# Kernel optimization log

Hardware: AMD Instinct MI355X
Metric: run time of the kernel (lower is better)

## Reference

```python
import jax, jax.numpy as jnp
import numpy as np

B, S, D = 4, 512, 4096
H, G = 32, 8           # num_heads, num_groups (GQA)
HD = D // H            # head_dim = 128
REP = H // G           # query heads per kv group = 4


def rotate_half(x):
    x1, x2 = x[..., : x.shape[-1] // 2], x[..., x.shape[-1] // 2 :]
    return jnp.concatenate([-x2, x1], axis=-1)


def setup_inputs() -> dict:
    key = jax.random.key(0)
    ks = jax.random.split(key, 5)
    return {
        "x": jax.random.normal(ks[0], (B, S, D), dtype=jnp.float32),
        "wq": jax.random.normal(ks[1], (D, D), dtype=jnp.float32) * 0.02,
        "bq": jnp.zeros((D,), dtype=jnp.float32),
        "wk": jax.random.normal(ks[2], (D, G * HD), dtype=jnp.float32) * 0.02,
        "bk": jnp.zeros((G * HD,), dtype=jnp.float32),
        "wv": jax.random.normal(ks[3], (D, G * HD), dtype=jnp.float32) * 0.02,
        "bv": jnp.zeros((G * HD,), dtype=jnp.float32),
        "wo": jax.random.normal(ks[4], (D, D), dtype=jnp.float32) * 0.02,
        "bo": jnp.zeros((D,), dtype=jnp.float32),
    }


def reference(x, wq, bq, wk, bk, wv, bv, wo, bo):
    b, s, d = x.shape
    q = (x @ wq + bq).reshape(b, s, H, HD)
    k = (x @ wk + bk).reshape(b, s, G, HD)
    v = (x @ wv + bv).reshape(b, s, G, HD)

    # RoPE tables (identical to module's cached sin/cos, sliced to seq len)
    inv_freq = 1.0 / (10000.0 ** (jnp.arange(0, HD, 2, dtype=jnp.float32) / HD))
    freqs = jnp.outer(jnp.arange(s, dtype=jnp.float32), inv_freq)  # [s, HD/2]
    freqs = jnp.concatenate([freqs, freqs], axis=-1)               # [s, HD]
    sin = jnp.sin(freqs)[:, None, :]  # [s, 1, HD] broadcast over heads
    cos = jnp.cos(freqs)[:, None, :]

    q = q * cos + rotate_half(q) * sin
    k = k * cos + rotate_half(k) * sin

    # Module scales q by HD**-0.5 AND jax.nn.dot_product_attention applies its
    # own default 1/sqrt(HD) -> net logit scale is HD**-1. Reproduce exactly.
    scale = HD ** (-0.5)
    q = q * scale

    # GQA without materializing repeated k/v: group query heads.
    qg = q.reshape(b, s, G, REP, HD)
    logits = jnp.einsum("bqgrd,bkgd->bgrqk", qg, k) * scale  # second scale (SDPA default)
    attn = jax.nn.softmax(logits, axis=-1)
    out = jnp.einsum("bgrqk,bkgd->bqgrd", attn, v).reshape(b, s, d)
    return out @ wo + bo
```

## Files before the change

kernel.cpp:

```cpp
#include <hip/hip_runtime.h>
#include <math.h>

typedef unsigned short ushort_t;
typedef __attribute__((ext_vector_type(8))) short bf16x8;
typedef __attribute__((ext_vector_type(4))) float f32x4;
typedef __attribute__((ext_vector_type(4))) unsigned short us4;
typedef __attribute__((ext_vector_type(8))) unsigned short us8;

#define B_   4
#define S_   512
#define D_   4096
#define H_   32
#define G_   8
#define HD_  128
#define KV_  1024
#define M_   (B_ * S_)
#define QN_  6144

__device__ __forceinline__ float bf2f(ushort_t u) {
    union { unsigned u; float f; } x; x.u = ((unsigned)u) << 16; return x.f;
}
__device__ __forceinline__ ushort_t f2bf(float f) {
    union { float f; unsigned u; } x; x.f = f;
    unsigned r = x.u + 0x7fffu + ((x.u >> 16) & 1u);
    return (ushort_t)(r >> 16);
}

typedef const __attribute__((address_space(1))) void* gptr_t;
typedef __attribute__((address_space(3))) void* ldsptr_t;

__device__ __forceinline__ void gload_lds16(const void* g, void* lds) {
    __builtin_amdgcn_global_load_lds((gptr_t)g, (ldsptr_t)lds, 16, 0, 0);
}

#define BAR() asm volatile("s_barrier" ::: "memory")

__global__ void xconv(const float* __restrict__ x, ushort_t* __restrict__ xb, int n8)
{
    const int i = blockIdx.x * blockDim.x + threadIdx.x;
    if (i >= n8) return;
    const float4 a = *(const float4*)&x[(size_t)i * 8];
    const float4 b = *(const float4*)&x[(size_t)i * 8 + 4];
    us8 o;
    o[0] = f2bf(a.x); o[1] = f2bf(a.y); o[2] = f2bf(a.z); o[3] = f2bf(a.w);
    o[4] = f2bf(b.x); o[5] = f2bf(b.y); o[6] = f2bf(b.z); o[7] = f2bf(b.w);
    *(us8*)&xb[(size_t)i * 8] = o;
}

__global__ __launch_bounds__(256) void wconv_all(
    const float* __restrict__ wq, const float* __restrict__ wk,
    const float* __restrict__ wv, ushort_t* __restrict__ Wt)
{
    __shared__ float t[32][33];
    const int n0 = blockIdx.x * 32, k0 = blockIdx.y * 32;
    const float* W; int nsrc, N;
    if (n0 < 4096)      { W = wq; nsrc = n0;        N = 4096; }
    else if (n0 < 5120) { W = wk; nsrc = n0 - 4096; N = 1024; }
    else                { W = wv; nsrc = n0 - 5120; N = 1024; }
    const int tid = threadIdx.x;
    const int r = tid >> 3, c4 = (tid & 7) * 4;
    const float4 v = *(const float4*)&W[(size_t)(k0 + r) * N + nsrc + c4];
    t[r][c4 + 0] = v.x; t[r][c4 + 1] = v.y; t[r][c4 + 2] = v.z; t[r][c4 + 3] = v.w;
    __syncthreads();
    us4 o;
    o.x = f2bf(t[c4 + 0][r]);
    o.y = f2bf(t[c4 + 1][r]);
    o.z = f2bf(t[c4 + 2][r]);
    o.w = f2bf(t[c4 + 3][r]);
    *(us4*)&Wt[(size_t)(n0 + r) * D_ + k0 + c4] = o;
}

__global__ __launch_bounds__(256) void wconv(
    const float* __restrict__ W, ushort_t* __restrict__ Wt, int K, int N)
{
    __shared__ float t[32][33];
    const int n0 = blockIdx.x * 32, k0 = blockIdx.y * 32;
    const int tid = threadIdx.x;
    const int r = tid >> 3, c4 = (tid & 7) * 4;
    const float4 v = *(const float4*)&W[(size_t)(k0 + r) * N + n0 + c4];
    t[r][c4 + 0] = v.x; t[r][c4 + 1] = v.y; t[r][c4 + 2] = v.z; t[r][c4 + 3] = v.w;
    __syncthreads();
    us4 o;
    o.x = f2bf(t[c4 + 0][r]);
    o.y = f2bf(t[c4 + 1][r]);
    o.z = f2bf(t[c4 + 2][r]);
    o.w = f2bf(t[c4 + 3][r]);
    *(us4*)&Wt[(size_t)(n0 + r) * K + k0 + c4] = o;
}

template<int OUT_BF16, int SPLITK, int ROPE>
__global__ __launch_bounds__(512, 2) void gemm8(
    const ushort_t* __restrict__ A, int lda,
    const ushort_t* __restrict__ Bt, int ldb,
    const float* __restrict__ bias0, const float* __restrict__ bias1,
    const float* __restrict__ bias2,
    float* __restrict__ Cf, ushort_t* __restrict__ Cb,
    float* __restrict__ P0, float* __restrict__ P1,
    int M, int N, int K)
{
    __shared__ ushort_t sA[2][256 * 64];
    __shared__ ushort_t sB[2][256 * 64];

    const int tid = threadIdx.x;
    const int lane = tid & 63, w = tid >> 6;
    const int lr = lane & 15, kg = lane >> 4;
    const int wr = w >> 2, wc = w & 3;

    const int nwg = gridDim.x;
    const int cpx = nwg >> 3;
    const int bid = (blockIdx.x & 7) * cpx + (blockIdx.x >> 3);
    int khalf = 0, tile = bid;
    if (SPLITK) { khalf = bid >> 7; tile = bid & 127; }
    const int nbx = N >> 8;
    const int bx = tile % nbx, by = tile / nbx;
    const int bm0 = by << 8, bn0 = bx << 8;
    if (SPLITK) { A += (size_t)khalf * K; Bt += (size_t)khalf * K; }

    const int NT = K >> 6;

    auto stage = [&](int t, int h) {
        const int c = t & 1;
        const ushort_t* gb; int ld; char* sbase;
        if (h < 2) { gb = A + (size_t)bm0 * lda; ld = lda; sbase = (char*)sA; }
        else       { gb = Bt + (size_t)bn0 * ldb; ld = ldb; sbase = (char*)sB; }
        const int half = h & 1;
        #pragma unroll
        for (int j = 0; j < 2; ++j) {
            const int o = j * 8192 + tid * 16;
            const int row = half * 128 + (o >> 7);
            const int slot = (o >> 4) & 7;
            gload_lds16(gb + (size_t)row * ld + t * 64 + ((slot ^ (row & 7)) << 3),
                        sbase + c * 32768 + half * 16384 + j * 8192 + w * 1024);
        }
    };
    auto lda_frag = [&](int c, int mi, int s) {
        const int row = mi * 32 + wr * 16 + lr;
        return *(const bf16x8*)((const char*)sA + c * 32768 + row * 128 +
                                (((s * 4 + kg) ^ (row & 7)) << 4));
    };
    auto ldb_frag = [&](int c, int ni, int s) {
        const int row = ni * 64 + wc * 16 + lr;
        return *(const bf16x8*)((const char*)sB + c * 32768 + row * 128 +
                                (((s * 4 + kg) ^ (row & 7)) << 4));
    };

    f32x4 acc[8][4];
    #pragma unroll
    for (int i = 0; i < 8; ++i)
        #pragma unroll
        for (int j = 0; j < 4; ++j)
            acc[i][j] = (f32x4){0.f, 0.f, 0.f, 0.f};

    stage(0, 0); stage(0, 2); stage(0, 3); stage(0, 1);
    stage(1, 0); stage(1, 2); stage(1, 3);
    asm volatile("s_waitcnt vmcnt(6)" ::: "memory");
    BAR();

    for (int t = 0; t < NT; ++t) {
        const int c = t & 1;
        bf16x8 a[4][2], b[4][2];

        #pragma unroll
        for (int ni = 0; ni < 2; ++ni)
            #pragma unroll
            for (int s = 0; s < 2; ++s) b[ni][s] = ldb_frag(c, ni, s);
        #pragma unroll
        for (int mi = 0; mi < 4; ++mi)
            #pragma unroll
            for (int s = 0; s < 2; ++s) a[mi][s] = lda_frag(c, mi, s);
        if (t + 1 < NT) stage(t + 1, 1);
        BAR();
        __builtin_amdgcn_s_setprio(1);
        #pragma unroll
        for (int mi = 0; mi < 4; ++mi)
            #pragma unroll
            for (int ni = 0; ni < 2; ++ni)
                #pragma unroll
                for (int s = 0; s < 2; ++s)
                    acc[mi][ni] = __builtin_amdgcn_mfma_f32_16x16x32_bf16(
                        a[mi][s], b[ni][s], acc[mi][ni], 0, 0, 0);
        __builtin_amdgcn_s_setprio(0);
        BAR();

        #pragma unroll
        for (int ni = 2; ni < 4; ++ni)
            #pragma unroll
            for (int s = 0; s < 2; ++s) b[ni][s] = ldb_frag(c, ni, s);
        if (t + 2 < NT) stage(t + 2, 0);
        BAR();
        __builtin_amdgcn_s_setprio(1);
        #pragma unroll
        for (int mi = 0; mi < 4; ++mi)
            #pragma unroll
            for (int ni = 2; ni < 4; ++ni)
                #pragma unroll
                for (int s = 0; s < 2; ++s)
                    acc[mi][ni] = __builtin_amdgcn_mfma_f32_16x16x32_bf16(
                        a[mi][s], b[ni][s], acc[mi][ni], 0, 0, 0);
        __builtin_amdgcn_s_setprio(0);
        BAR();

        #pragma unroll
        for (int mi = 0; mi < 4; ++mi)
            #pragma unroll
            for (int s = 0; s < 2; ++s) a[mi][s] = lda_frag(c, mi + 4, s);
        if (t + 2 < NT) stage(t + 2, 2);
        BAR();
        __builtin_amdgcn_s_setprio(1);
        #pragma unroll
        for (int mi = 0; mi < 4; ++mi)
            #pragma unroll
            for (int ni = 2; ni < 4; ++ni)
                #pragma unroll
                for (int s = 0; s < 2; ++s)
                    acc[mi + 4][ni] = __builtin_amdgcn_mfma_f32_16x16x32_bf16(
                        a[mi][s], b[ni][s], acc[mi + 4][ni], 0, 0, 0);
        __builtin_amdgcn_s_setprio(0);
        BAR();

        if (t + 2 < NT) {
            stage(t + 2, 3);
            asm volatile("s_waitcnt vmcnt(6)" ::: "memory");
        } else {
            asm volatile("s_waitcnt vmcnt(0)" ::: "memory");
        }
        BAR();
        __builtin_amdgcn_s_setprio(1);
        #pragma unroll
        for (int mi = 0; mi < 4; ++mi)
            #pragma unroll
            for (int ni = 0; ni < 2; ++ni)
                #pragma unroll
                for (int s = 0; s < 2; ++s)
                    acc[mi + 4][ni] = __builtin_amdgcn_mfma_f32_16x16x32_bf16(
                        a[mi][s], b[ni][s], acc[mi + 4][ni], 0, 0, 0);
        __builtin_amdgcn_s_setprio(0);
        BAR();
    }

    if (ROPE && bn0 < 5120) {
        const float scale = (bn0 < 4096) ? (1.f / 128.f) : 1.f;
        const int jj = wc * 16 + lr;
        const float invf = __expf(-0.1439115683121279f * (float)jj);
        #pragma unroll
        for (int mi = 0; mi < 8; ++mi) {
            const int mr = bm0 + mi * 32 + wr * 16 + kg * 4;
            #pragma unroll
            for (int r = 0; r < 4; ++r) {
                const int srow = (mr + r) & 511;
                float sn, cs;
                __sincosf((float)srow * invf, &sn, &cs);
                #pragma unroll
                for (int nip = 0; nip < 2; ++nip) {
                    const int n_lo = bn0 + nip * 128 + jj;
                    const int n_hi = n_lo + 64;
                    const float b_lo = (n_lo < 4096) ? bias0[n_lo]
                                     : (n_lo < 5120) ? bias1[n_lo - 4096] : bias2[n_lo - 5120];
                    const float b_hi = (n_hi < 4096) ? bias0[n_hi]
                                     : (n_hi < 5120) ? bias1[n_hi - 4096] : bias2[n_hi - 5120];
                    const float a_lo = acc[mi][nip * 2][r] + b_lo;
                    const float a_hi = acc[mi][nip * 2 + 1][r] + b_hi;
                    Cb[(size_t)(mr + r) * N + n_lo] = f2bf((a_lo * cs - a_hi * sn) * scale);
                    Cb[(size_t)(mr + r) * N + n_hi] = f2bf((a_hi * cs + a_lo * sn) * scale);
                }
            }
        }
        return;
    }
    #pragma unroll
    for (int mi = 0; mi < 8; ++mi) {
        #pragma unroll
        for (int ni = 0; ni < 4; ++ni) {
            const int n = bn0 + ni * 64 + wc * 16 + lr;
            const float bs = (n < 4096) ? bias0[n]
                           : (n < 5120) ? bias1[n - 4096] : bias2[n - 5120];
            const int mr = bm0 + mi * 32 + wr * 16 + kg * 4;
            #pragma unroll
            for (int r = 0; r < 4; ++r) {
                if (SPLITK) {
                    const int row = mr + r;
                    if (khalf == 0) {
                        Cf[(size_t)row * N + n] = acc[mi][ni][r] + bs;
                    } else {
                        float* P = (row < 1024) ? P0 : P1;
                        P[((size_t)(row & 1023) << 12) + n] = acc[mi][ni][r];
                    }
                } else {
                    const float val = acc[mi][ni][r] + bs;
                    if (OUT_BF16) Cb[(size_t)(mr + r) * N + n] = f2bf(val);
                    else          Cf[(size_t)(mr + r) * N + n] = val;
                }
            }
        }
    }
}

__global__ void reduce_add(const float* __restrict__ P0, const float* __restrict__ P1,
                           float* __restrict__ out)
{
    const int n4 = M_ * D_ / 4;
    for (int i4 = blockIdx.x * blockDim.x + threadIdx.x; i4 < n4;
         i4 += gridDim.x * blockDim.x) {
        const float4 p = (i4 < (1 << 20))
            ? *(const float4*)&P0[(size_t)i4 * 4]
            : *(const float4*)&P1[(size_t)(i4 - (1 << 20)) * 4];
        float4 o = *(float4*)&out[(size_t)i4 * 4];
        o.x += p.x; o.y += p.y; o.z += p.z; o.w += p.w;
        *(float4*)&out[(size_t)i4 * 4] = o;
    }
}

__global__ __launch_bounds__(256) void vtrans(
    const ushort_t* __restrict__ vb,
    ushort_t* __restrict__ vT)
{
    __shared__ ushort_t t[32][40];
    const int s0 = blockIdx.x * 32;
    const int d0 = blockIdx.y * 32;
    const int bg = blockIdx.z;
    const int b = bg >> 3, g = bg & 7;
    const int tid = threadIdx.x;
    const int row = tid >> 3, c4 = (tid & 7) * 4;
    const us4 v = *(const us4*)&vb[(size_t)(b * S_ + s0 + row) * QN_ + g * HD_ + d0 + c4];
    t[row][c4 + 0] = v.x; t[row][c4 + 1] = v.y;
    t[row][c4 + 2] = v.z; t[row][c4 + 3] = v.w;
    __syncthreads();
    us4 o;
    o.x = t[c4 + 0][row]; o.y = t[c4 + 1][row];
    o.z = t[c4 + 2][row]; o.w = t[c4 + 3][row];
    *(us4*)&vT[(size_t)(bg * HD_ + d0 + row) * S_ + s0 + c4] = o;
}

__global__ __launch_bounds__(256) void attn_mfma(
    const ushort_t* __restrict__ kb,
    const ushort_t* __restrict__ vT,
    ushort_t* __restrict__ qb)
{
    __shared__ ushort_t sKV[8192];
    __shared__ ushort_t sP[4 * 16 * 512];

    const int q0 = blockIdx.x * 64;
    const int h = blockIdx.y, b = blockIdx.z;
    const int g = h >> 2;
    const int tid = threadIdx.x;
    const int lane = tid & 63, w = tid >> 6;
    const int lr = lane & 15, kg = lane >> 4;

    bf16x8 af[4];
    {
        const ushort_t* qrow = qb + (size_t)(b * S_ + q0 + w * 16 + lr) * QN_ + h * HD_;
        #pragma unroll
        for (int c = 0; c < 4; ++c)
            af[c] = *(const bf16x8*)(qrow + c * 32 + kg * 8);
    }

    f32x4 l[8][4];
    #pragma unroll
    for (int ch = 0; ch < 8; ++ch)
        #pragma unroll
        for (int t = 0; t < 4; ++t)
            l[ch][t] = (f32x4){0.f, 0.f, 0.f, 0.f};

    const ushort_t* kbase = kb + (size_t)b * S_ * QN_ + g * HD_;
    #pragma unroll
    for (int ch = 0; ch < 8; ++ch) {
        __syncthreads();
        #pragma unroll
        for (int i = 0; i < 4; ++i) {
            const int o = w * 4096 + i * 1024;
            const int key = (o >> 8) + (lane >> 4);
            const int sl = lane & 15;
            gload_lds16(kbase + (size_t)(ch * 64 + key) * QN_ + ((sl ^ (key & 15)) * 8),
                        (char*)sKV + o);
        }
        __syncthreads();
        #pragma unroll
        for (int t = 0; t < 4; ++t) {
            const int key = t * 16 + lr;
            #pragma unroll
            for (int c = 0; c < 4; ++c) {
                const bf16x8 bf = *(const bf16x8*)((const char*)sKV + key * 256 +
                                                   (((c * 4 + kg) ^ (key & 15)) << 4));
                l[ch][t] = __builtin_amdgcn_mfma_f32_16x16x32_bf16(af[c], bf, l[ch][t], 0, 0, 0);
            }
        }
    }

    float inv[4];
    #pragma unroll
    for (int r = 0; r < 4; ++r) {
        float m = -1e30f;
        #pragma unroll
        for (int ch = 0; ch < 8; ++ch)
            #pragma unroll
            for (int t = 0; t < 4; ++t)
                m = fmaxf(m, l[ch][t][r]);
        #pragma unroll
        for (int msk = 1; msk <= 8; msk <<= 1)
            m = fmaxf(m, __shfl_xor(m, msk));
        float s = 0.f;
        const int q = kg * 4 + r;
        #pragma unroll
        for (int ch = 0; ch < 8; ++ch)
            #pragma unroll
            for (int t = 0; t < 4; ++t) {
                const float p = __expf(l[ch][t][r] - m);
                s += p;
                const int gs = ch * 8 + t * 2 + (lr >> 3);
                sP[w * 8192 + q * 512 + ((gs ^ q) << 3) + (lr & 7)] = f2bf(p);
            }
        #pragma unroll
        for (int msk = 1; msk <= 8; msk <<= 1)
            s += __shfl_xor(s, msk);
        inv[r] = 1.f / s;
    }

    f32x4 oacc[8];
    #pragma unroll
    for (int dt = 0; dt < 8; ++dt) oacc[dt] = (f32x4){0.f, 0.f, 0.f, 0.f};

    const ushort_t* vbase = vT + (size_t)(b * G_ + g) * HD_ * S_;
    for (int ch = 0; ch < 8; ++ch) {
        __syncthreads();
        #pragma unroll
        for (int i = 0; i < 4; ++i) {
            const int o = w * 4096 + i * 1024;
            const int d = (o >> 7) + (lane >> 3);
            const int sl = lane & 7;
            gload_lds16(vbase + (size_t)d * S_ + ch * 64 + ((sl ^ (d & 7)) * 8),
                        (char*)sKV + o);
        }
        __syncthreads();
        #pragma unroll
        for (int c2 = 0; c2 < 2; ++c2) {
            const int gs = ch * 8 + c2 * 4 + kg;
            const bf16x8 ap = *(const bf16x8*)((const char*)sP + w * 16384 + lr * 1024 +
                                               ((gs ^ lr) << 4));
            #pragma unroll
            for (int dt = 0; dt < 8; ++dt) {
                const int d = dt * 16 + lr;
                const bf16x8 bv = *(const bf16x8*)((const char*)sKV + d * 128 +
                                                   (((c2 * 4 + kg) ^ (d & 7)) << 4));
                oacc[dt] = __builtin_amdgcn_mfma_f32_16x16x32_bf16(ap, bv, oacc[dt], 0, 0, 0);
            }
        }
    }

    #pragma unroll
    for (int dt = 0; dt < 8; ++dt) {
        #pragma unroll
        for (int r = 0; r < 4; ++r) {
            const int q = kg * 4 + r;
            qb[(size_t)(b * S_ + q0 + w * 16 + q) * QN_ + h * HD_ + dt * 16 + lr] =
                f2bf(oacc[dt][r] * inv[r]);
        }
    }
}

extern "C" void kernel_launch(void* const* d_in, const int* in_sizes, int n_in,
                              void* d_out, int out_size, void* d_ws, size_t ws_size,
                              hipStream_t stream)
{
    const float* x  = (const float*)d_in[0];
    const float* wq = (const float*)d_in[1];
    const float* bq = (const float*)d_in[2];
    const float* wk = (const float*)d_in[3];
    const float* bk = (const float*)d_in[4];
    const float* wv = (const float*)d_in[5];
    const float* bv = (const float*)d_in[6];
    const float* wo = (const float*)d_in[7];
    const float* bo = (const float*)d_in[8];
    float* out = (float*)d_out;

    char* ws = (char*)d_ws;
    ushort_t* xb   = (ushort_t*)(ws);
    ushort_t* Wt   = (ushort_t*)(ws + (16u << 20));
    ushort_t* vT   = (ushort_t*)(ws + (48u << 20));
    ushort_t* qkv  = (ushort_t*)(ws + (64u << 20));
    float* p0      = (float*)xb;
    float* p1      = (float*)(ws + (48u << 20));

    wconv_all<<<dim3(QN_ / 32, D_ / 32), 256, 0, stream>>>(wq, wk, wv, Wt);
    xconv<<<(M_ * D_ / 8 + 255) / 256, 256, 0, stream>>>(x, xb, M_ * D_ / 8);

    gemm8<1, 0, 1><<<(QN_ / 256) * (M_ / 256), 512, 0, stream>>>(
        xb, D_, Wt, D_, bq, bk, bv, nullptr, qkv, nullptr, nullptr, M_, QN_, D_);

    vtrans<<<dim3(S_ / 32, HD_ / 32, B_ * G_), 256, 0, stream>>>(qkv + 5120, vT);

    attn_mfma<<<dim3(S_ / 64, H_, B_), 256, 0, stream>>>(qkv + 4096, vT, qkv);

    wconv<<<dim3(D_ / 32, D_ / 32), 256, 0, stream>>>(wo, Wt, D_, D_);

    gemm8<0, 1, 0><<<256, 512, 0, stream>>>(
        qkv, QN_, Wt, D_, bo, bo, bo, out, nullptr, p0, p1, M_, D_, 2048);
    reduce_add<<<2048, 256, 0, stream>>>(p0, p1, out);
}
```

Baseline: 312.9 us.

## Double-buffer K/V LDS loads in attention and precompute GEMM staging addresses

```diff
diff --git a/kernel.cpp b/kernel.cpp
--- a/kernel.cpp
+++ b/kernel.cpp
@@ -118,8 +118,10 @@
 
     const int NT = K >> 6;
 
-    auto stage = [&](int t, int h) {
-        const int c = t & 1;
+    const ushort_t* gp[4][2];
+    char*           lp[4][2];
+    #pragma unroll
+    for (int h = 0; h < 4; ++h) {
         const ushort_t* gb; int ld; char* sbase;
         if (h < 2) { gb = A + (size_t)bm0 * lda; ld = lda; sbase = (char*)sA; }
         else       { gb = Bt + (size_t)bn0 * ldb; ld = ldb; sbase = (char*)sB; }
@@ -129,9 +131,14 @@
             const int o = j * 8192 + tid * 16;
             const int row = half * 128 + (o >> 7);
             const int slot = (o >> 4) & 7;
-            gload_lds16(gb + (size_t)row * ld + t * 64 + ((slot ^ (row & 7)) << 3),
-                        sbase + c * 32768 + half * 16384 + j * 8192 + w * 1024);
-        }
+            gp[h][j] = gb + (size_t)row * ld + ((slot ^ (row & 7)) << 3);
+            lp[h][j] = sbase + half * 16384 + j * 8192 + w * 1024;
+        }
+    }
+    auto stage = [&](int t, int h, int c) {
+        #pragma unroll
+        for (int j = 0; j < 2; ++j)
+            gload_lds16(gp[h][j] + t * 64, lp[h][j] + c * 32768);
     };
     auto lda_frag = [&](int c, int mi, int s) {
         const int row = mi * 32 + wr * 16 + lr;
@@ -151,13 +158,12 @@
         for (int j = 0; j < 4; ++j)
             acc[i][j] = (f32x4){0.f, 0.f, 0.f, 0.f};
 
-    stage(0, 0); stage(0, 2); stage(0, 3); stage(0, 1);
-    stage(1, 0); stage(1, 2); stage(1, 3);
+    stage(0, 0, 0); stage(0, 2, 0); stage(0, 3, 0); stage(0, 1, 0);
+    stage(1, 0, 1); stage(1, 2, 1); stage(1, 3, 1);
     asm volatile("s_waitcnt vmcnt(6)" ::: "memory");
     BAR();
 
-    for (int t = 0; t < NT; ++t) {
-        const int c = t & 1;
+    auto iter = [&](int t, int c) {
         bf16x8 a[4][2], b[4][2];
 
         #pragma unroll
@@ -168,7 +174,7 @@
         for (int mi = 0; mi < 4; ++mi)
             #pragma unroll
             for (int s = 0; s < 2; ++s) a[mi][s] = lda_frag(c, mi, s);
-        if (t + 1 < NT) stage(t + 1, 1);
+        if (t + 1 < NT) stage(t + 1, 1, c ^ 1);
         BAR();
         __builtin_amdgcn_s_setprio(1);
         #pragma unroll
@@ -186,7 +192,7 @@
         for (int ni = 2; ni < 4; ++ni)
             #pragma unroll
             for (int s = 0; s < 2; ++s) b[ni][s] = ldb_frag(c, ni, s);
-        if (t + 2 < NT) stage(t + 2, 0);
+        if (t + 2 < NT) stage(t + 2, 0, c);
         BAR();
         __builtin_amdgcn_s_setprio(1);
         #pragma unroll
@@ -204,7 +210,7 @@
         for (int mi = 0; mi < 4; ++mi)
             #pragma unroll
             for (int s = 0; s < 2; ++s) a[mi][s] = lda_frag(c, mi + 4, s);
-        if (t + 2 < NT) stage(t + 2, 2);
+        if (t + 2 < NT) stage(t + 2, 2, c);
         BAR();
         __builtin_amdgcn_s_setprio(1);
         #pragma unroll
@@ -219,7 +225,7 @@
         BAR();
 
         if (t + 2 < NT) {
-            stage(t + 2, 3);
+            stage(t + 2, 3, c);
             asm volatile("s_waitcnt vmcnt(6)" ::: "memory");
         } else {
             asm volatile("s_waitcnt vmcnt(0)" ::: "memory");
@@ -236,7 +242,9 @@
                         a[mi][s], b[ni][s], acc[mi + 4][ni], 0, 0, 0);
         __builtin_amdgcn_s_setprio(0);
         BAR();
-    }
+    };
+
+    for (int t = 0; t < NT; t += 2) { iter(t, 0); iter(t + 1, 1); }
 
     if (ROPE && bn0 < 5120) {
         const float scale = (bn0 < 4096) ? (1.f / 128.f) : 1.f;
@@ -336,7 +344,7 @@
     const ushort_t* __restrict__ vT,
     ushort_t* __restrict__ qb)
 {
-    __shared__ ushort_t sKV[8192];
+    __shared__ ushort_t sKV[2][8192];
     __shared__ ushort_t sP[4 * 16 * 512];
 
     const int q0 = blockIdx.x * 64;
@@ -354,37 +362,63 @@
             af[c] = *(const bf16x8*)(qrow + c * 32 + kg * 8);
     }
 
-    f32x4 l[8][4];
-    #pragma unroll
-    for (int ch = 0; ch < 8; ++ch)
-        #pragma unroll
-        for (int t = 0; t < 4; ++t)
-            l[ch][t] = (f32x4){0.f, 0.f, 0.f, 0.f};
-
     const ushort_t* kbase = kb + (size_t)b * S_ * QN_ + g * HD_;
-    #pragma unroll
-    for (int ch = 0; ch < 8; ++ch) {
-        __syncthreads();
+    const ushort_t* vbase = vT + (size_t)(b * G_ + g) * HD_ * S_;
+
+    auto kstage = [&](int ch, int buf) {
         #pragma unroll
         for (int i = 0; i < 4; ++i) {
             const int o = w * 4096 + i * 1024;
             const int key = (o >> 8) + (lane >> 4);
             const int sl = lane & 15;
             gload_lds16(kbase + (size_t)(ch * 64 + key) * QN_ + ((sl ^ (key & 15)) * 8),
-                        (char*)sKV + o);
-        }
-        __syncthreads();
+                        (char*)sKV + buf * 16384 + o);
+        }
+    };
+    auto vstage = [&](int ch, int buf) {
+        #pragma unroll
+        for (int i = 0; i < 4; ++i) {
+            const int o = w * 4096 + i * 1024;
+            const int d = (o >> 7) + (lane >> 3);
+            const int sl = lane & 7;
+            gload_lds16(vbase + (size_t)d * S_ + ch * 64 + ((sl ^ (d & 7)) * 8),
+                        (char*)sKV + buf * 16384 + o);
+        }
+    };
+
+    f32x4 l[8][4];
+    #pragma unroll
+    for (int ch = 0; ch < 8; ++ch)
+        #pragma unroll
+        for (int t = 0; t < 4; ++t)
+            l[ch][t] = (f32x4){0.f, 0.f, 0.f, 0.f};
+
+    kstage(0, 0);
+    #pragma unroll
+    for (int ch = 0; ch < 8; ++ch) {
+        const int buf = ch & 1;
+        if (ch < 7) {
+            kstage(ch + 1, buf ^ 1);
+            asm volatile("s_waitcnt vmcnt(4)" ::: "memory");
+        } else {
+            asm volatile("s_waitcnt vmcnt(0)" ::: "memory");
+        }
+        BAR();
         #pragma unroll
         for (int t = 0; t < 4; ++t) {
             const int key = t * 16 + lr;
             #pragma unroll
             for (int c = 0; c < 4; ++c) {
-                const bf16x8 bf = *(const bf16x8*)((const char*)sKV + key * 256 +
+                const bf16x8 bf = *(const bf16x8*)((const char*)sKV + buf * 16384 +
+                                                   key * 256 +
                                                    (((c * 4 + kg) ^ (key & 15)) << 4));
                 l[ch][t] = __builtin_amdgcn_mfma_f32_16x16x32_bf16(af[c], bf, l[ch][t], 0, 0, 0);
             }
         }
-    }
+        BAR();
+    }
+
+    vstage(0, 0);
 
     float inv[4];
     #pragma unroll
@@ -419,18 +453,16 @@
     #pragma unroll
     for (int dt = 0; dt < 8; ++dt) oacc[dt] = (f32x4){0.f, 0.f, 0.f, 0.f};
 
-    const ushort_t* vbase = vT + (size_t)(b * G_ + g) * HD_ * S_;
+    #pragma unroll
     for (int ch = 0; ch < 8; ++ch) {
-        __syncthreads();
-        #pragma unroll
-        for (int i = 0; i < 4; ++i) {
-            const int o = w * 4096 + i * 1024;
-            const int d = (o >> 7) + (lane >> 3);
-            const int sl = lane & 7;
-            gload_lds16(vbase + (size_t)d * S_ + ch * 64 + ((sl ^ (d & 7)) * 8),
-                        (char*)sKV + o);
-        }
-        __syncthreads();
+        const int buf = ch & 1;
+        if (ch < 7) {
+            vstage(ch + 1, buf ^ 1);
+            asm volatile("s_waitcnt vmcnt(4)" ::: "memory");
+        } else {
+            asm volatile("s_waitcnt vmcnt(0)" ::: "memory");
+        }
+        BAR();
         #pragma unroll
         for (int c2 = 0; c2 < 2; ++c2) {
             const int gs = ch * 8 + c2 * 4 + kg;
@@ -439,11 +471,13 @@
             #pragma unroll
             for (int dt = 0; dt < 8; ++dt) {
                 const int d = dt * 16 + lr;
-                const bf16x8 bv = *(const bf16x8*)((const char*)sKV + d * 128 +
+                const bf16x8 bv = *(const bf16x8*)((const char*)sKV + buf * 16384 +
+                                                   d * 128 +
                                                    (((c2 * 4 + kg) ^ (d & 7)) << 4));
                 oacc[dt] = __builtin_amdgcn_mfma_f32_16x16x32_bf16(ap, bv, oacc[dt], 0, 0, 0);
             }
         }
+        BAR();
     }
 
     #pragma unroll
```

Result: slower. 327.5 us (+4.7%).
